# Kernel optimization log

Hardware: AMD Instinct MI355X
Metric: run time of the kernel (lower is better)

Reference implementation:

```python
import jax, jax.numpy as jnp
import numpy as np

# Config mirroring RegionExtractor(__init__ defaults, stage='rcnn')
MIN_SIZE = 25.0
IOU_THRESH = 0.3
SCORE_THRESH = 0.001  # applied as box_score_thresh inside the wrapped FRCNN
MAX_DET = 100         # max_detections_per_image
IMG_SIZE = 800.0
B, N = 8, 2048


def setup_inputs() -> dict:
    key = jax.random.key(0)
    k_c, k_wh, k_s = jax.random.split(key, 3)
    # synthesize realistic xyxy boxes inside an 800x800 image
    centers = jax.random.uniform(k_c, (B, N, 2), minval=0.0, maxval=IMG_SIZE)
    wh = jax.random.uniform(k_wh, (B, N, 2), minval=1.0, maxval=250.0)
    x1y1 = jnp.clip(centers - wh / 2, 0.0, IMG_SIZE)
    x2y2 = jnp.clip(centers + wh / 2, 0.0, IMG_SIZE)
    boxes = jnp.concatenate([x1y1, x2y2], axis=-1).astype(jnp.float32)  # [B,N,4]
    scores = jax.random.uniform(k_s, (B, N), dtype=jnp.float32)          # [B,N]
    return {"boxes": boxes, "scores": scores}


def _box_iou(a, b):
    # a: [N,4], b: [N,4] xyxy -> [N,N] IoU (torchvision convention, no +1)
    area_a = (a[:, 2] - a[:, 0]) * (a[:, 3] - a[:, 1])
    area_b = (b[:, 2] - b[:, 0]) * (b[:, 3] - b[:, 1])
    lt = jnp.maximum(a[:, None, :2], b[None, :, :2])
    rb = jnp.minimum(a[:, None, 2:], b[None, :, 2:])
    wh = jnp.clip(rb - lt, 0.0)
    inter = wh[..., 0] * wh[..., 1]
    return inter / (area_a[:, None] + area_b[None, :] - inter)


def _process_image(boxes, scores):
    # boxes [N,4], scores [N] -> (out [K,4], mask [K])
    n = boxes.shape[0]
    w = boxes[:, 2] - boxes[:, 0]
    h = boxes[:, 3] - boxes[:, 1]
    # remove_small_boxes + score threshold (box_score_thresh in wrapped FRCNN)
    valid = (w >= MIN_SIZE) & (h >= MIN_SIZE) & (scores >= SCORE_THRESH)
    order = jnp.argsort(-jnp.where(valid, scores, -jnp.inf))  # desc, invalid last
    b = boxes[order]
    v = valid[order]
    sup = _box_iou(b, b) > IOU_THRESH  # [N,N]
    idx = jnp.arange(n)

    def body(i, keep):
        suppressed = jnp.any(keep & sup[:, i] & (idx < i))
        return keep.at[i].set(v[i] & ~suppressed)

    keep = jax.lax.fori_loop(0, n, body, jnp.zeros(n, dtype=bool))
    # keep is in score order already; take first MAX_DET kept boxes
    rank = jnp.cumsum(keep) - 1
    sel = keep & (rank < MAX_DET)
    tgt = jnp.where(sel, rank, MAX_DET)  # dump non-selected into scratch row
    out = jnp.zeros((MAX_DET + 1, 4), boxes.dtype).at[tgt].set(b)[:MAX_DET]
    num_kept = jnp.minimum(jnp.sum(keep), MAX_DET)
    mask = jnp.arange(MAX_DET) < num_kept
    return out, mask


def reference(boxes, scores):
    # Per-image filter + NMS + top-k, batched via vmap (padded fixed-shape output:
    # original returns a ragged [sum_k,5]; here rows with mask==False are padding).
    out, mask = jax.vmap(_process_image)(boxes, scores)  # [B,K,4], [B,K]
    b = boxes.shape[0]
    img_idx = jnp.repeat(jnp.arange(b, dtype=boxes.dtype), MAX_DET)[:, None]  # [B*K,1]
    regions = jnp.concatenate([img_idx, out.reshape(b * MAX_DET, 4)], axis=1)  # [B*K,5]
    return regions, mask.reshape(-1)
```

## Files before the change

kernel.cpp:

```cpp
#include <hip/hip_runtime.h>

#define NBOX   2048
#define HALF   1024
#define MAXDET 100
#define NIMG   8
#define POOL   256
#define IOU_MID 0x1.333335p-2

typedef unsigned long long u64;

__device__ __forceinline__ u64 shx64(u64 v, int m) {
    int lo = __shfl_xor((int)(unsigned int)v, m, 64);
    int hi = __shfl_xor((int)(unsigned int)(v >> 32), m, 64);
    return ((u64)(unsigned int)hi << 32) | (unsigned int)lo;
}
__device__ __forceinline__ u64 cmpsel(u64 mine, u64 part, bool take_max) {
    return ((mine > part) == take_max) ? mine : part;
}
__device__ __forceinline__ u64 readlane64(u64 v, int l) {
    unsigned int lo = (unsigned int)__builtin_amdgcn_readlane((int)(unsigned int)v, l);
    unsigned int hi = (unsigned int)__builtin_amdgcn_readlane((int)(v >> 32), l);
    return ((u64)hi << 32) | lo;
}
__device__ __forceinline__ u64 mkkey(float4 v, float s, int i) {
    bool valid = ((v.z - v.x) >= 25.0f) && ((v.w - v.y) >= 25.0f) && (s >= 0.001f);
    unsigned int sk = valid ? __float_as_uint(s) : 0u;
    return ((u64)sk << 32) | (unsigned int)(~i);
}

__global__ __launch_bounds__(512) void k_all(
    const float* __restrict__ boxes, const float* __restrict__ scores,
    float* __restrict__ out)
{
    __shared__ u64    bufA[NBOX];
    __shared__ u64    bufB[NBOX];
    __shared__ u64    supRow[POOL * 4];
    __shared__ float4 sbox[POOL];
    __shared__ u64    mA[POOL], mB[POOL];
    __shared__ u64    validW[4];
    __shared__ u64    pminS;
    __shared__ int    kposL[MAXDET];
    __shared__ float4 leadersB[MAXDET];
    __shared__ float  leadersA[MAXDET];

    const int g    = threadIdx.x;
    const int lane = g & 63;
    const int wv   = g >> 6;
    const int img  = blockIdx.x;
    const float4* bb4 = (const float4*)boxes + img * NBOX;
    const float*  ss  = scores + img * NBOX;

    const int e0 = 2 * g;
    u64 k0, k1, k2, k3;
    { float4 v = bb4[e0];            k0 = mkkey(v, ss[e0],            e0);            }
    { float4 v = bb4[e0 + 1];        k1 = mkkey(v, ss[e0 + 1],        e0 + 1);        }
    { float4 v = bb4[HALF + e0];     k2 = mkkey(v, ss[HALF + e0],     HALF + e0);     }
    { float4 v = bb4[HALF + e0 + 1]; k3 = mkkey(v, ss[HALF + e0 + 1], HALF + e0 + 1); }

#define SWAP1(a, b, D) { if ((D) ? ((a) < (b)) : ((a) > (b))) { u64 t_ = (a); (a) = (b); (b) = t_; } }
    { bool D = ((g & 1) == 0); SWAP1(k0, k1, D) SWAP1(k2, k3, D) }
    for (int KB = 2; KB <= 64; KB <<= 1) {
        bool D = ((g & KB) == 0);
        for (int m = KB >> 1; m >= 1; m >>= 1) {
            bool tm = (D == ((lane & m) == 0));
            k0 = cmpsel(k0, shx64(k0, m), tm);
            k1 = cmpsel(k1, shx64(k1, m), tm);
            k2 = cmpsel(k2, shx64(k2, m), tm);
            k3 = cmpsel(k3, shx64(k3, m), tm);
        }
        SWAP1(k0, k1, D) SWAP1(k2, k3, D)
    }
    int sp = 0;
    for (int K = 256; K <= 1024; K <<= 1) {
        bool D = ((e0 & K) == 0);
        for (int j = K >> 1; j >= 128; j >>= 1) {
            u64* buf = (sp & 1) ? bufB : bufA;
            ++sp;
            buf[e0] = k0;        buf[e0 + 1] = k1;
            buf[HALF + e0] = k2; buf[HALF + e0 + 1] = k3;
            __syncthreads();
            int pe = e0 ^ j;
            u64 p0 = buf[pe], p1 = buf[pe + 1];
            u64 p2 = buf[HALF + pe], p3 = buf[HALF + pe + 1];
            bool tm = (D == ((e0 & j) == 0));
            k0 = cmpsel(k0, p0, tm); k1 = cmpsel(k1, p1, tm);
            k2 = cmpsel(k2, p2, tm); k3 = cmpsel(k3, p3, tm);
        }
        for (int m = 32; m >= 1; m >>= 1) {
            bool tm = (D == ((lane & m) == 0));
            k0 = cmpsel(k0, shx64(k0, m), tm);
            k1 = cmpsel(k1, shx64(k1, m), tm);
            k2 = cmpsel(k2, shx64(k2, m), tm);
            k3 = cmpsel(k3, shx64(k3, m), tm);
        }
        SWAP1(k0, k1, D) SWAP1(k2, k3, D)
    }
    bufA[e0] = k0;        bufA[e0 + 1] = k1;
    bufA[HALF + e0] = k2; bufA[HALF + e0 + 1] = k3;
    __syncthreads();

    const u64* hk = bufA;

    u64 c = 0;
    if (g < POOL) {
        u64 a  = hk[g];
        u64 bq = hk[HALF + (POOL - 1 - g)];
        c = (a > bq) ? a : bq;
        mA[g] = c;
    }
    __syncthreads();
    if (g < POOL) { c = cmpsel(c, mA[g ^ 128], (g & 128) == 0); mB[g] = c; }
    __syncthreads();
    if (g < POOL) {
        c = cmpsel(c, mB[g ^ 64], (g & 64) == 0);
        for (int m = 32; m >= 1; m >>= 1)
            c = cmpsel(c, shx64(c, m), (lane & m) == 0);
        unsigned int idx = ~(unsigned int)c;
        float4 v = bb4[idx];
        sbox[g] = v;
        u64 bal = __ballot(((unsigned int)(c >> 32)) != 0u);
        if (lane == 0) validW[wv] = bal;
        if (g == POOL - 1) pminS = c;
    }
    __syncthreads();

    float4 cb[4];
    float  ca[4];
#pragma unroll
    for (int w = 0; w < 4; ++w) {
        float4 v = sbox[(w << 6) + lane];
        cb[w] = v;
        ca[w] = (v.z - v.x) * (v.w - v.y);
    }

    for (int r = 0; r < POOL / 8; ++r) {
        int i = (r << 3) + wv;
        float4 Li = sbox[i];
        float La = (Li.z - Li.x) * (Li.w - Li.y);
        int w0 = i >> 6;
#pragma unroll
        for (int w = 0; w < 4; ++w) {
            if (w >= w0) {
                int j0 = (w << 6) + lane;
                float iw = fminf(Li.z, cb[w].z) - fmaxf(Li.x, cb[w].x);
                float ih = fminf(Li.w, cb[w].w) - fmaxf(Li.y, cb[w].y);
                iw = fmaxf(iw, 0.0f);
                ih = fmaxf(ih, 0.0f);
                float inter = iw * ih;
                float denom = (La + ca[w]) - inter;
                bool hit = (j0 > i) && ((double)inter > IOU_MID * (double)denom);
                u64 bits = __ballot(hit);
                if (lane == 0) supRow[(i << 2) + w] = bits;
            }
        }
    }
    __syncthreads();

    if (g >= 64) return;

    float* regions = out;
    float* maskv   = out + (size_t)NIMG * MAXDET * 5;

    u64 rd0 = supRow[(((0 << 6) + lane) << 2) + 0];
    u64 rd1 = supRow[(((1 << 6) + lane) << 2) + 1];
    u64 rd2 = supRow[(((2 << 6) + lane) << 2) + 2];
    u64 rd3 = supRow[(((3 << 6) + lane) << 2) + 3];

    int nkept = 0;
    u64 pend = 0;
#pragma unroll
    for (int s = 0; s < 4; ++s) {
        u64 rds = (s == 0) ? rd0 : (s == 1) ? rd1 : (s == 2) ? rd2 : rd3;
        u64 mcur = validW[s] & ~readlane64(pend, s);
        int n0 = nkept;
        while (mcur != 0ULL) {
            int il = (int)__builtin_ctzll(mcur);
            if (lane == 0) kposL[nkept] = (s << 6) + il;
            nkept++;
            if (nkept >= MAXDET) break;
            u64 rowS = readlane64(rds, il);
            mcur = (mcur & (mcur - 1)) & ~rowS;
        }
        if (nkept >= MAXDET) break;
        if (s < 3) {
            for (int t = n0 + (lane >> 2); t < nkept; t += 16)
                pend |= supRow[(kposL[t] << 2) + (lane & 3)];
            pend |= shx64(pend, 4);
            pend |= shx64(pend, 8);
            pend |= shx64(pend, 16);
            pend |= shx64(pend, 32);
        }
    }

    for (int t = lane; t < nkept; t += 64) {
        int ip = kposL[t];
        float4 v = sbox[ip];
        float* rr = regions + ((size_t)(img * MAXDET + t)) * 5;
        rr[0] = (float)img; rr[1] = v.x; rr[2] = v.y; rr[3] = v.z; rr[4] = v.w;
        maskv[img * MAXDET + t] = 1.0f;
        leadersB[t] = v;
        leadersA[t] = (v.z - v.x) * (v.w - v.y);
    }

    if (nkept < MAXDET) {
        u64 pmin = pminS;
        int q0 = 0, q1 = 0;
        while (q0 < HALF && hk[q0] >= pmin) ++q0;
        while (q1 < HALF && hk[HALF + q1] >= pmin) ++q1;
        while (nkept < MAXDET) {
            u64 h0 = (q0 < HALF) ? hk[q0] : 0;
            u64 h1 = (q1 < HALF) ? hk[HALF + q1] : 0;
            u64 hmax = (h0 > h1) ? h0 : h1;
            if ((unsigned int)(hmax >> 32) == 0u) break;
            if (hmax == h0) ++q0; else ++q1;
            unsigned int idx = ~(unsigned int)hmax;
            float4 v = bb4[idx];
            float varea = (v.z - v.x) * (v.w - v.y);
            bool sup = false;
            for (int t = lane; t < nkept; t += 64) {
                float4 Lb = leadersB[t];
                float  La = leadersA[t];
                float iw = fminf(Lb.z, v.z) - fmaxf(Lb.x, v.x);
                float ih = fminf(Lb.w, v.w) - fmaxf(Lb.y, v.y);
                iw = fmaxf(iw, 0.0f);
                ih = fmaxf(ih, 0.0f);
                float inter = iw * ih;
                float denom = (La + varea) - inter;
                if ((double)inter > IOU_MID * (double)denom) sup = true;
            }
            if (__ballot(sup) == 0ULL) {
                if (lane == 0) {
                    float* rr = regions + ((size_t)(img * MAXDET + nkept)) * 5;
                    rr[0] = (float)img; rr[1] = v.x; rr[2] = v.y; rr[3] = v.z; rr[4] = v.w;
                    maskv[img * MAXDET + nkept] = 1.0f;
                    leadersB[nkept] = v;
                    leadersA[nkept] = varea;
                }
                nkept++;
            }
        }
    }

    for (int r = nkept + lane; r < MAXDET; r += 64) {
        float* rr = regions + ((size_t)(img * MAXDET + r)) * 5;
        rr[0] = (float)img; rr[1] = 0.0f; rr[2] = 0.0f; rr[3] = 0.0f; rr[4] = 0.0f;
        maskv[img * MAXDET + r] = 0.0f;
    }
}

extern "C" void kernel_launch(void* const* d_in, const int* in_sizes, int n_in,
                              void* d_out, int out_size, void* d_ws, size_t ws_size,
                              hipStream_t stream) {
    const float* boxes  = (const float*)d_in[0];
    const float* scores = (const float*)d_in[1];
    float* out = (float*)d_out;
    k_all<<<NIMG, 512, 0, stream>>>(boxes, scores, out);
}
```

Baseline: 83.29 us.

## Batch fallback NMS over 64 merged candidates per wave instead of one-at-a-time

The serial fallback loop took one candidate per iteration from two sorted halves and checked it against the kept leaders across lanes. Now each lane uses merge-path binary search to pick the next 64 candidates in merged order. Each lane tests its own candidate against all leaders, and survivors are then resolved in order among themselves with ballots. The pool-boundary scan is also replaced by ballot popcounts. This cuts the number of serialized iterations at the cost of per-lane leader loops and extra shuffles.

```diff
diff --git a/kernel.cpp b/kernel.cpp
--- a/kernel.cpp
+++ b/kernel.cpp
@@ -205,19 +205,42 @@
     if (nkept < MAXDET) {
         u64 pmin = pminS;
         int q0 = 0, q1 = 0;
-        while (q0 < HALF && hk[q0] >= pmin) ++q0;
-        while (q1 < HALF && hk[HALF + q1] >= pmin) ++q1;
-        while (nkept < MAXDET) {
-            u64 h0 = (q0 < HALF) ? hk[q0] : 0;
-            u64 h1 = (q1 < HALF) ? hk[HALF + q1] : 0;
-            u64 hmax = (h0 > h1) ? h0 : h1;
-            if ((unsigned int)(hmax >> 32) == 0u) break;
-            if (hmax == h0) ++q0; else ++q1;
-            unsigned int idx = ~(unsigned int)hmax;
-            float4 v = bb4[idx];
-            float varea = (v.z - v.x) * (v.w - v.y);
-            bool sup = false;
-            for (int t = lane; t < nkept; t += 64) {
+#pragma unroll
+        for (int w = 0; w < 16; ++w) {
+            q0 += __popcll(__ballot(hk[(w << 6) + lane] >= pmin));
+            q1 += __popcll(__ballot(hk[HALF + (w << 6) + lane] >= pmin));
+        }
+        for (;;) {
+            const int lenA = HALF - q0, lenB = HALF - q1;
+            const int rem  = lenA + lenB;
+            if (rem <= 0) break;
+            u64  myKey = 0;
+            bool fromA = false;
+            if (lane < rem) {
+                int lo = lane + 1 - lenB; if (lo < 0) lo = 0;
+                int hi = (lane + 1 < lenA) ? lane + 1 : lenA;
+                while (lo < hi) {
+                    int a = (lo + hi) >> 1, b = lane + 1 - a;
+                    if (a < lenA && b > 0 && hk[q0 + a] > hk[HALF + q1 + b - 1]) lo = a + 1;
+                    else hi = a;
+                }
+                int a = lo, b = lane + 1 - a;
+                u64 ka = (a > 0) ? hk[q0 + a - 1] : ~0ULL;
+                u64 kb = (b > 0) ? hk[HALF + q1 + b - 1] : ~0ULL;
+                fromA = (ka < kb);
+                myKey = fromA ? ka : kb;
+            }
+            bool validC = (lane < rem) && (((unsigned int)(myKey >> 32)) != 0u);
+            u64 vmask = __ballot(validC);
+            float4 v = make_float4(0.0f, 0.0f, 0.0f, 0.0f);
+            float varea = 0.0f;
+            if (validC) {
+                v = bb4[~(unsigned int)myKey];
+                varea = (v.z - v.x) * (v.w - v.y);
+            }
+            bool supL = false;
+#pragma unroll 4
+            for (int t = 0; t < nkept; ++t) {
                 float4 Lb = leadersB[t];
                 float  La = leadersA[t];
                 float iw = fminf(Lb.z, v.z) - fmaxf(Lb.x, v.x);
@@ -226,10 +249,15 @@
                 ih = fmaxf(ih, 0.0f);
                 float inter = iw * ih;
                 float denom = (La + varea) - inter;
-                if ((double)inter > IOU_MID * (double)denom) sup = true;
-            }
-            if (__ballot(sup) == 0ULL) {
-                if (lane == 0) {
+                supL = supL || ((double)inter > IOU_MID * (double)denom);
+            }
+            u64 mcur = vmask & ~__ballot(supL);
+            while (mcur != 0ULL) {
+                int il = (int)__builtin_ctzll(mcur);
+                float bx = __shfl(v.x, il, 64), by = __shfl(v.y, il, 64);
+                float bz = __shfl(v.z, il, 64), bw = __shfl(v.w, il, 64);
+                float ba = __shfl(varea, il, 64);
+                if (lane == il) {
                     float* rr = regions + ((size_t)(img * MAXDET + nkept)) * 5;
                     rr[0] = (float)img; rr[1] = v.x; rr[2] = v.y; rr[3] = v.z; rr[4] = v.w;
                     maskv[img * MAXDET + nkept] = 1.0f;
@@ -237,7 +265,22 @@
                     leadersA[nkept] = varea;
                 }
                 nkept++;
-            }
+                if (nkept >= MAXDET) break;
+                float iw = fminf(bz, v.z) - fmaxf(bx, v.x);
+                float ih = fminf(bw, v.w) - fmaxf(by, v.y);
+                iw = fmaxf(iw, 0.0f);
+                ih = fmaxf(ih, 0.0f);
+                float inter = iw * ih;
+                float denom = (ba + varea) - inter;
+                bool hit = ((double)inter > IOU_MID * (double)denom);
+                mcur = (mcur & (mcur - 1)) & ~__ballot(hit);
+            }
+            if (nkept >= MAXDET) break;
+            int nv = __popcll(vmask);
+            if (nv < 64) break;
+            int nA = __popcll(vmask & __ballot(fromA));
+            q0 += nA;
+            q1 += nv - nA;
         }
     }
 
```

Measured after the change: 83.66 us. About the same (+0.5%).
